# Kernel tuning notes

Hardware: AMD Instinct MI355X
Metric: run time of the kernel (lower is better)

Reference implementation:

```python
import jax, jax.numpy as jnp
import numpy as np

N, E, D, G, S, H = 100000, 1600000, 64, 1024, 4096, 128
BN_EPS = 1e-5


def setup_inputs() -> dict:
    key = jax.random.key(0)
    ks = jax.random.split(key, 24)
    x = jax.random.normal(ks[0], (N, D), jnp.float32)
    sid = jax.random.randint(ks[1], (N,), 0, S)
    x = x.at[:, 5].set(sid.astype(jnp.float32))  # column 5 holds integer substructure ids
    edge_index = jax.random.randint(ks[2], (2, E), 0, N, dtype=jnp.int32)
    batch = jnp.sort(jax.random.randint(ks[3], (N,), 0, G, dtype=jnp.int32))

    def lin(k, fan_in, shape):
        return jax.random.normal(k, shape, jnp.float32) / np.sqrt(fan_in)

    return {
        "x": x, "edge_index": edge_index, "batch": batch,
        # substructure attention net: Linear(D,64) -> tanh -> Linear(64,1,no bias)
        "w1": lin(ks[4], D, (D, 64)), "b1": jnp.zeros((64,), jnp.float32),
        "w2": lin(ks[5], 64, (64,)),
        "cw0": lin(ks[6], D + 1, (D + 1, H)), "cb0": jnp.zeros((H,), jnp.float32),
        "cw_rest": lin(ks[7], H, (3, H, H)), "cb_rest": jnp.zeros((3, H), jnp.float32),
        # BatchNorm1d (eval mode: running stats)
        "bn_gamma": jnp.ones((4, H), jnp.float32), "bn_beta": jnp.zeros((4, H), jnp.float32),
        "bn_mean": 0.1 * jax.random.normal(ks[8], (4, H), jnp.float32),
        "bn_var": jax.random.uniform(ks[9], (4, H), jnp.float32, 0.5, 1.5),
        # pred head: Linear(128,64) -> ELU -> Linear(64,1)
        "hw1": lin(ks[10], H, (H, 64)), "hb1": jnp.zeros((64,), jnp.float32),
        "hw2": lin(ks[11], 64, (64, 1)), "hb2": jnp.zeros((1,), jnp.float32),
    }


def _subst_attention(x, subst_ids, w1, b1, w2):
    ones = jnp.ones((x.shape[0],), x.dtype)
    cnt = jax.ops.segment_sum(ones, subst_ids, num_segments=S)
    sums = jax.ops.segment_sum(x, subst_ids, num_segments=S)
    means = sums / jnp.maximum(cnt, 1.0)[:, None]          # [S, D] per-substructure mean
    scores = jnp.tanh(means @ w1 + b1) @ w2                # [S]
    attn = jax.nn.softmax(scores, axis=0)                  # softmax over substructures
    return attn[subst_ids][:, None]                        # [N, 1] broadcast back to atoms


def _gcn(x, W, b, row, col, norm, n):
    h = x @ W                                              # [N, H]
    msg = h[row] * norm[:, None]                           # gather + scale  [E+N, H]
    return jax.ops.segment_sum(msg, col, num_segments=n) + b


def reference(x, edge_index, batch, w1, b1, w2, cw0, cb0, cw_rest, cb_rest,
              bn_gamma, bn_beta, bn_mean, bn_var, hw1, hb1, hw2, hb2):
    n = x.shape[0]
    subst_ids = jax.lax.stop_gradient(x[:, 5]).astype(jnp.int32)
    attn = _subst_attention(x, subst_ids, w1, b1, w2)
    h = jnp.concatenate([x, attn], axis=1)                 # [N, D+1]

    # add self loops, symmetric GCN normalization (as in PyG GCNConv)
    loops = jnp.arange(n, dtype=edge_index.dtype)
    row = jnp.concatenate([edge_index[0], loops])
    col = jnp.concatenate([edge_index[1], loops])
    deg = jax.ops.segment_sum(jnp.ones_like(row, dtype=h.dtype), col, num_segments=n)
    dinv = jax.lax.rsqrt(jnp.maximum(deg, 1.0))
    norm = dinv[row] * dinv[col]

    def bn(z, i):
        return (z - bn_mean[i]) * jax.lax.rsqrt(bn_var[i] + BN_EPS) * bn_gamma[i] + bn_beta[i]

    h = jax.nn.elu(bn(_gcn(h, cw0, cb0, row, col, norm, n), 0))
    for i in range(3):
        z = bn(_gcn(h, cw_rest[i], cb_rest[i], row, col, norm, n), i + 1)
        h = jax.nn.elu(z) if i < 2 else jax.nn.relu(z)

    # global mean pool over graphs
    gcnt = jax.ops.segment_sum(jnp.ones((n,), h.dtype), batch, num_segments=G)
    pooled = jax.ops.segment_sum(h, batch, num_segments=G) / jnp.maximum(gcnt, 1.0)[:, None]

    return jax.nn.elu(pooled @ hw1 + hb1) @ hw2 + hb2      # [G, 1]
```

## Files before the change

kernel.cpp:

```cpp
#include <hip/hip_runtime.h>
#include <math.h>

static constexpr int SS = 4096;
static constexpr int HH = 128;
static constexpr float EPS_BN = 1e-5f;

typedef __attribute__((ext_vector_type(8))) short bf16x8;
typedef __attribute__((ext_vector_type(4))) float f32x4;

__device__ inline unsigned short f2bf(float f) {
  unsigned int u = __float_as_uint(f);
  return (unsigned short)((u + 0x7fffu + ((u >> 16) & 1u)) >> 16);
}
__device__ inline float bflo(unsigned int u) { return __uint_as_float(u << 16); }
__device__ inline float bfhi(unsigned int u) { return __uint_as_float(u & 0xffff0000u); }


__device__ void wpack_body(const float* __restrict__ W, unsigned short* __restrict__ out,
                           int nkc, int idx) {
  if (idx >= 8 * nkc * 64) return;
  int lane = idx & 63;
  int kc = (idx >> 6) % nkc;
  int nt = idx / (64 * nkc);
  int colc = nt * 16 + (lane & 15);
  int k0 = kc * 32 + (lane >> 4) * 8;
  unsigned int w[4];
  #pragma unroll
  for (int i = 0; i < 4; ++i) {
    unsigned short a = f2bf(W[(size_t)(k0 + 2 * i) * 128 + colc]);
    unsigned short b = f2bf(W[(size_t)(k0 + 2 * i + 1) * 128 + colc]);
    w[i] = (unsigned int)a | ((unsigned int)b << 16);
  }
  *(uint4*)&out[(size_t)idx * 8] = make_uint4(w[0], w[1], w[2], w[3]);
}

__global__ __launch_bounds__(256)
void gcn_front1(const int* __restrict__ col, int* __restrict__ fill, int* __restrict__ pos,
                const float* __restrict__ x, float* __restrict__ cnt, float* __restrict__ sums,
                unsigned int* __restrict__ xh, const int* __restrict__ batch,
                int* __restrict__ gstart,
                const float* __restrict__ cw0, const float* __restrict__ cwr,
                unsigned short* __restrict__ wpk0, unsigned short* __restrict__ wpkr,
                const float* __restrict__ cb0, const float* __restrict__ cbr,
                const float* __restrict__ bng, const float* __restrict__ bnb,
                const float* __restrict__ bnm, const float* __restrict__ bnv,
                float* __restrict__ bnS, float* __restrict__ bnT,
                int n, int e, int G,
                int nbPos, int nbSub, int nbXb, int nbGb, int nbW0, int nbWr) {
  int b = blockIdx.x;
  int t = threadIdx.x;
  if (b < nbPos) {
    int i = b * 256 + t;
    if (i < e) pos[i] = atomicAdd(&fill[col[i]], 1);
    return;
  }
  b -= nbPos;
  if (b < nbSub) {
    int node = b * 4 + (t >> 6);
    int lane = t & 63;
    if (node >= n) return;
    const float* xr = x + (size_t)node * 64;
    float v = xr[lane];
    int sid = (int)__shfl(v, 5, 64);
    if (lane == 0) atomicAdd(&cnt[sid], 1.0f);
    atomicAdd(&sums[(size_t)sid * 64 + lane], v);
    return;
  }
  b -= nbSub;
  if (b < nbXb) {
    int i = b * 256 + t;
    if (i >= n * 32) return;
    int pr = i & 31;
    float2 v = *(const float2*)&x[(size_t)(i >> 5) * 64 + pr * 2];
    if (pr == 2) v.y = 0.f;
    xh[i] = (unsigned int)f2bf(v.x) | ((unsigned int)f2bf(v.y) << 16);
    return;
  }
  b -= nbXb;
  if (b < nbGb) {
    int g = b * 256 + t;
    if (g > G) return;
    if (g == G) { gstart[G] = n; return; }
    int lo = 0, hi = n;
    while (lo < hi) { int mid = (lo + hi) >> 1; if (batch[mid] < g) lo = mid + 1; else hi = mid; }
    gstart[g] = lo;
    return;
  }
  b -= nbGb;
  if (b < nbW0) { wpack_body(cw0, wpk0, 2, b * 256 + t); return; }
  b -= nbW0;
  if (b < 3 * nbWr) {
    int l = b / nbWr, bb = b % nbWr;
    wpack_body(cwr + (size_t)l * HH * HH, wpkr + (size_t)l * 8 * 4 * 64 * 8, 4, bb * 256 + t);
    return;
  }
  b -= 3 * nbWr;
  {
    int i = b * 256 + t;
    if (i >= 512) return;
    int l = i >> 7, c = i & 127;
    float S = rsqrtf(bnv[i] + EPS_BN) * bng[i];
    float bias = (l == 0) ? cb0[c] : cbr[(l - 1) * 128 + c];
    bnS[i] = S;
    bnT[i] = fmaf(bias - bnm[i], S, bnb[i]);
  }
}


__global__ void gcn_scores(const float* __restrict__ sums, const float* __restrict__ cnt,
                           const float* __restrict__ w1, const float* __restrict__ b1,
                           const float* __restrict__ w2, float* __restrict__ scores) {
  int s = blockIdx.x * 4 + (threadIdx.x >> 6);
  int j = threadIdx.x & 63;
  float r = 1.0f / fmaxf(cnt[s], 1.0f);
  const float* ss = sums + (size_t)s * 64;
  float acc = b1[j];
  #pragma unroll 8
  for (int d = 0; d < 64; ++d) acc = fmaf(ss[d] * r, w1[d * 64 + j], acc);
  float t = tanhf(acc) * w2[j];
  #pragma unroll
  for (int off = 32; off; off >>= 1) t += __shfl_down(t, off, 64);
  if (j == 0) scores[s] = t;
}

__global__ void gcn_softmax(float* __restrict__ sc) {
  int t = threadIdx.x;
  int wid = t >> 6;
  float v[4]; float m = -INFINITY;
  for (int i = 0; i < 4; ++i) { v[i] = sc[t + i * 1024]; m = fmaxf(m, v[i]); }
  for (int off = 32; off; off >>= 1) m = fmaxf(m, __shfl_xor(m, off, 64));
  __shared__ float wmax[16];
  if ((t & 63) == 0) wmax[wid] = m;
  __syncthreads();
  if (t == 0) { float mm = wmax[0]; for (int i = 1; i < 16; ++i) mm = fmaxf(mm, wmax[i]); wmax[0] = mm; }
  __syncthreads();
  float M = wmax[0];
  float s = 0.f;
  for (int i = 0; i < 4; ++i) { v[i] = expf(v[i] - M); s += v[i]; }
  for (int off = 32; off; off >>= 1) s += __shfl_xor(s, off, 64);
  __shared__ float wsum[16];
  if ((t & 63) == 0) wsum[wid] = s;
  __syncthreads();
  if (t == 0) { float ts = 0.f; for (int i = 0; i < 16; ++i) ts += wsum[i]; wsum[0] = ts; }
  __syncthreads();
  float inv = 1.0f / wsum[0];
  for (int i = 0; i < 4; ++i) sc[t + i * 1024] = v[i] * inv;
}


__global__ void gcn_scan1(const int* __restrict__ fill, int* __restrict__ rowstart,
                          int* __restrict__ bsum, float* __restrict__ dinv, int n) {
  __shared__ int tmp[1024];
  int t = threadIdx.x; int g = blockIdx.x * 1024 + t;
  int v = (g < n) ? fill[g] : 0;
  if (g < n) dinv[g] = rsqrtf((float)v + 1.0f);
  tmp[t] = v; __syncthreads();
  for (int off = 1; off < 1024; off <<= 1) {
    int a = (t >= off) ? tmp[t - off] : 0; __syncthreads();
    tmp[t] += a; __syncthreads();
  }
  if (g < n) rowstart[g] = tmp[t] - v;
  if (t == 1023) bsum[blockIdx.x] = tmp[t];
}

__global__ void gcn_scan2(int* __restrict__ bsum, int nb) {
  __shared__ int tmp[128];
  int t = threadIdx.x;
  int v = (t < nb) ? bsum[t] : 0;
  tmp[t] = v; __syncthreads();
  for (int off = 1; off < 128; off <<= 1) {
    int a = (t >= off) ? tmp[t - off] : 0; __syncthreads();
    tmp[t] += a; __syncthreads();
  }
  if (t < nb) bsum[t] = tmp[t] - v;
}

__global__ void gcn_scan3(int* __restrict__ rowstart, const int* __restrict__ bsum, int n, int e) {
  int g = blockIdx.x * 1024 + threadIdx.x;
  if (g < n) rowstart[g] += bsum[blockIdx.x];
  if (g == 0) rowstart[n] = e;
}


__global__ __launch_bounds__(256)
void gcn_front3(const float* __restrict__ x, const float* __restrict__ attn,
                float2* __restrict__ np,
                const int* __restrict__ row, const int* __restrict__ col,
                const int* __restrict__ pos, const int* __restrict__ rowstart,
                const float* __restrict__ dinv, int2* __restrict__ sedge,
                int n, int e, int nbNp) {
  int b = blockIdx.x;
  int t = threadIdx.x;
  if (b < nbNp) {
    int i = b * 256 + t;
    if (i >= n) return;
    int sid = (int)x[(size_t)i * 64 + 5];
    np[i] = make_float2((float)sid, attn[sid]);
    return;
  }
  b -= nbNp;
  int i = b * 256 + t;
  if (i >= e) return;
  int c = col[i], r = row[i];
  sedge[rowstart[c] + pos[i]] = make_int2(r, __float_as_int(dinv[r] * dinv[c]));
}


__global__ __launch_bounds__(256)
void gcn_layer_f(const unsigned short* __restrict__ hIn, const int2* __restrict__ sedge,
                 const int* __restrict__ rowstart, const float* __restrict__ dinv,
                 const unsigned short* __restrict__ Wpk,
                 const float* __restrict__ bnS, const float* __restrict__ bnT,
                 unsigned short* __restrict__ hOut, int relu, int n) {
  __shared__ unsigned short tile[4][16][136];
  int t = threadIdx.x;
  int wid = t >> 6, l = t & 63;
  int r = l & 15, kg = l >> 4;
  size_t row0w = (size_t)blockIdx.x * 64 + wid * 16;
  int noderaw = (int)row0w + r;
  bool valid = noderaw < n;
  int node = valid ? noderaw : n - 1;
  float di = dinv[node], d2 = di * di;
  const uint4* h4 = (const uint4*)hIn;
  float a[4][8];
  #pragma unroll
  for (int kc = 0; kc < 4; ++kc) {
    uint4 u = h4[(size_t)node * 16 + kc * 4 + kg];
    a[kc][0] = bflo(u.x) * d2; a[kc][1] = bfhi(u.x) * d2;
    a[kc][2] = bflo(u.y) * d2; a[kc][3] = bfhi(u.y) * d2;
    a[kc][4] = bflo(u.z) * d2; a[kc][5] = bfhi(u.z) * d2;
    a[kc][6] = bflo(u.w) * d2; a[kc][7] = bfhi(u.w) * d2;
  }
  int s_ = valid ? rowstart[node] : 0;
  int e_ = valid ? rowstart[node + 1] : 0;
  int2 se = (s_ < e_) ? sedge[s_] : make_int2(0, 0);
  for (int j = s_; j < e_; ++j) {
    int2 cur = se;
    if (j + 1 < e_) se = sedge[j + 1];
    float w = __int_as_float(cur.y);
    #pragma unroll
    for (int kc = 0; kc < 4; ++kc) {
      uint4 u = h4[(size_t)cur.x * 16 + kc * 4 + kg];
      a[kc][0] = fmaf(bflo(u.x), w, a[kc][0]); a[kc][1] = fmaf(bfhi(u.x), w, a[kc][1]);
      a[kc][2] = fmaf(bflo(u.y), w, a[kc][2]); a[kc][3] = fmaf(bfhi(u.y), w, a[kc][3]);
      a[kc][4] = fmaf(bflo(u.z), w, a[kc][4]); a[kc][5] = fmaf(bfhi(u.z), w, a[kc][5]);
      a[kc][6] = fmaf(bflo(u.w), w, a[kc][6]); a[kc][7] = fmaf(bfhi(u.w), w, a[kc][7]);
    }
  }
  bf16x8 af[4];
  #pragma unroll
  for (int kc = 0; kc < 4; ++kc) {
    uint4 pk;
    pk.x = (unsigned)f2bf(a[kc][0]) | ((unsigned)f2bf(a[kc][1]) << 16);
    pk.y = (unsigned)f2bf(a[kc][2]) | ((unsigned)f2bf(a[kc][3]) << 16);
    pk.z = (unsigned)f2bf(a[kc][4]) | ((unsigned)f2bf(a[kc][5]) << 16);
    pk.w = (unsigned)f2bf(a[kc][6]) | ((unsigned)f2bf(a[kc][7]) << 16);
    af[kc] = *(bf16x8*)&pk;
  }
  f32x4 acc[8];
  #pragma unroll
  for (int nt = 0; nt < 8; ++nt) acc[nt] = (f32x4){0.f, 0.f, 0.f, 0.f};
  const unsigned short* wp = Wpk + (size_t)l * 8;
  #pragma unroll
  for (int kc = 0; kc < 4; ++kc) {
    bf16x8 bf[8];
    #pragma unroll
    for (int nt = 0; nt < 8; ++nt)
      bf[nt] = *(const bf16x8*)(wp + (size_t)(nt * 4 + kc) * 512);
    #pragma unroll
    for (int nt = 0; nt < 8; ++nt)
      acc[nt] = __builtin_amdgcn_mfma_f32_16x16x32_bf16(af[kc], bf[nt], acc[nt], 0, 0, 0);
  }
  int colb = l & 15, rb = kg * 4;
  #pragma unroll
  for (int nt = 0; nt < 8; ++nt) {
    int c = nt * 16 + colb;
    float S = bnS[c], T = bnT[c];
    #pragma unroll
    for (int j = 0; j < 4; ++j) {
      float v = fmaf(acc[nt][j], S, T);
      v = relu ? fmaxf(v, 0.f) : (v > 0.f ? v : expf(v) - 1.f);
      tile[wid][rb + j][c] = f2bf(v);
    }
  }
  __syncthreads();
  #pragma unroll
  for (int i = 0; i < 4; ++i) {
    int m = i * 64 + l;
    int rr = m >> 4, chunk = m & 15;
    uint4 v = *(const uint4*)&tile[wid][rr][chunk * 8];
    *(uint4*)&hOut[(row0w + rr) * 128 + chunk * 8] = v;
  }
}


__global__ __launch_bounds__(256)
void gcn_layer0_f(const unsigned int* __restrict__ xh, const float2* __restrict__ np,
                  const int2* __restrict__ sedge, const int* __restrict__ rowstart,
                  const float* __restrict__ dinv, const unsigned short* __restrict__ Wpk0,
                  const float* __restrict__ cw0,
                  const float* __restrict__ bnS, const float* __restrict__ bnT,
                  unsigned short* __restrict__ hOut, int n) {
  __shared__ unsigned short tile[4][16][136];
  int t = threadIdx.x;
  int wid = t >> 6, l = t & 63;
  int r = l & 15, kg = l >> 4;
  size_t row0w = (size_t)blockIdx.x * 64 + wid * 16;
  int noderaw = (int)row0w + r;
  bool valid = noderaw < n;
  int node = valid ? noderaw : n - 1;
  float di = dinv[node], d2 = di * di;
  const uint4* x4 = (const uint4*)xh;
  float a[2][8];
  #pragma unroll
  for (int kc = 0; kc < 2; ++kc) {
    uint4 u = x4[(size_t)node * 8 + kc * 4 + kg];
    a[kc][0] = bflo(u.x) * d2; a[kc][1] = bfhi(u.x) * d2;
    a[kc][2] = bflo(u.y) * d2; a[kc][3] = bfhi(u.y) * d2;
    a[kc][4] = bflo(u.z) * d2; a[kc][5] = bfhi(u.z) * d2;
    a[kc][6] = bflo(u.w) * d2; a[kc][7] = bfhi(u.w) * d2;
  }
  float a5 = 0.f, a64 = 0.f;
  if (kg == 0) { float2 v = np[node]; a5 = d2 * v.x; a64 = d2 * v.y; }
  int s_ = valid ? rowstart[node] : 0;
  int e_ = valid ? rowstart[node + 1] : 0;
  int2 se = (s_ < e_) ? sedge[s_] : make_int2(0, 0);
  for (int j = s_; j < e_; ++j) {
    int2 cur = se;
    if (j + 1 < e_) se = sedge[j + 1];
    float w = __int_as_float(cur.y);
    #pragma unroll
    for (int kc = 0; kc < 2; ++kc) {
      uint4 u = x4[(size_t)cur.x * 8 + kc * 4 + kg];
      a[kc][0] = fmaf(bflo(u.x), w, a[kc][0]); a[kc][1] = fmaf(bfhi(u.x), w, a[kc][1]);
      a[kc][2] = fmaf(bflo(u.y), w, a[kc][2]); a[kc][3] = fmaf(bfhi(u.y), w, a[kc][3]);
      a[kc][4] = fmaf(bflo(u.z), w, a[kc][4]); a[kc][5] = fmaf(bfhi(u.z), w, a[kc][5]);
      a[kc][6] = fmaf(bflo(u.w), w, a[kc][6]); a[kc][7] = fmaf(bfhi(u.w), w, a[kc][7]);
    }
    if (kg == 0) {
      float2 v = np[cur.x];
      a5 = fmaf(v.x, w, a5);
      a64 = fmaf(v.y, w, a64);
    }
  }
  bf16x8 af[2];
  #pragma unroll
  for (int kc = 0; kc < 2; ++kc) {
    uint4 pk;
    pk.x = (unsigned)f2bf(a[kc][0]) | ((unsigned)f2bf(a[kc][1]) << 16);
    pk.y = (unsigned)f2bf(a[kc][2]) | ((unsigned)f2bf(a[kc][3]) << 16);
    pk.z = (unsigned)f2bf(a[kc][4]) | ((unsigned)f2bf(a[kc][5]) << 16);
    pk.w = (unsigned)f2bf(a[kc][6]) | ((unsigned)f2bf(a[kc][7]) << 16);
    af[kc] = *(bf16x8*)&pk;
  }
  f32x4 acc[8];
  #pragma unroll
  for (int nt = 0; nt < 8; ++nt) acc[nt] = (f32x4){0.f, 0.f, 0.f, 0.f};
  const unsigned short* wp = Wpk0 + (size_t)l * 8;
  #pragma unroll
  for (int kc = 0; kc < 2; ++kc) {
    bf16x8 bf[8];
    #pragma unroll
    for (int nt = 0; nt < 8; ++nt)
      bf[nt] = *(const bf16x8*)(wp + (size_t)(nt * 2 + kc) * 512);
    #pragma unroll
    for (int nt = 0; nt < 8; ++nt)
      acc[nt] = __builtin_amdgcn_mfma_f32_16x16x32_bf16(af[kc], bf[nt], acc[nt], 0, 0, 0);
  }
  int colb = l & 15, rb = kg * 4;
  float2 ax[4];
  #pragma unroll
  for (int j = 0; j < 4; ++j) {
    ax[j].x = __shfl(a5, rb + j, 64);
    ax[j].y = __shfl(a64, rb + j, 64);
  }
  #pragma unroll
  for (int nt = 0; nt < 8; ++nt) {
    int c = nt * 16 + colb;
    float w5 = cw0[5 * 128 + c], w64 = cw0[64 * 128 + c];
    float S = bnS[c], T = bnT[c];
    #pragma unroll
    for (int j = 0; j < 4; ++j) {
      float z = acc[nt][j] + ax[j].x * w5 + ax[j].y * w64;
      float v = fmaf(z, S, T);
      v = v > 0.f ? v : expf(v) - 1.f;
      tile[wid][rb + j][c] = f2bf(v);
    }
  }
  __syncthreads();
  #pragma unroll
  for (int i = 0; i < 4; ++i) {
    int m = i * 64 + l;
    int rr = m >> 4, chunk = m & 15;
    uint4 v = *(const uint4*)&tile[wid][rr][chunk * 8];
    *(uint4*)&hOut[(row0w + rr) * 128 + chunk * 8] = v;
  }
}


__global__ void gcn_pool2(const unsigned short* __restrict__ hB, const int* __restrict__ gstart,
                          float* __restrict__ pooled, int G) {
  int g = blockIdx.x * 4 + (threadIdx.x >> 6);
  int lane = threadIdx.x & 63;
  if (g >= G) return;
  int s = gstart[g], epos = gstart[g + 1];
  const unsigned int* h32 = (const unsigned int*)hB;
  float ax = 0.f, ay = 0.f;
  for (int i = s; i < epos; ++i) {
    unsigned int u = h32[(size_t)i * 64 + lane];
    ax += bflo(u);
    ay += bfhi(u);
  }
  float r = 1.0f / fmaxf((float)(epos - s), 1.0f);
  ((float2*)pooled)[(size_t)g * 64 + lane] = make_float2(ax * r, ay * r);
}

__global__ void gcn_head(const float* __restrict__ pooled,
                         const float* __restrict__ hw1, const float* __restrict__ hb1,
                         const float* __restrict__ hw2, const float* __restrict__ hb2,
                         float* __restrict__ out, int g) {
  int gi = blockIdx.x * 4 + (threadIdx.x >> 6);
  int j = threadIdx.x & 63;
  if (gi >= g) return;
  const float* p = pooled + (size_t)gi * 128;
  float acc = hb1[j];
  #pragma unroll 8
  for (int k = 0; k < 128; ++k) acc = fmaf(p[k], hw1[k * 64 + j], acc);
  float t = acc > 0.f ? acc : expf(acc) - 1.f;
  t *= hw2[j];
  #pragma unroll
  for (int off = 32; off; off >>= 1) t += __shfl_down(t, off, 64);
  if (j == 0) out[gi] = t + hb2[0];
}


extern "C" void kernel_launch(void* const* d_in, const int* in_sizes, int n_in,
                              void* d_out, int out_size, void* d_ws, size_t ws_size,
                              hipStream_t stream) {
  const float* x   = (const float*)d_in[0];
  const int*   ei  = (const int*)d_in[1];
  const int*   batch = (const int*)d_in[2];
  const float* w1  = (const float*)d_in[3];
  const float* b1  = (const float*)d_in[4];
  const float* w2  = (const float*)d_in[5];
  const float* cw0 = (const float*)d_in[6];
  const float* cb0 = (const float*)d_in[7];
  const float* cwr = (const float*)d_in[8];
  const float* cbr = (const float*)d_in[9];
  const float* bng = (const float*)d_in[10];
  const float* bnb = (const float*)d_in[11];
  const float* bnm = (const float*)d_in[12];
  const float* bnv = (const float*)d_in[13];
  const float* hw1 = (const float*)d_in[14];
  const float* hb1 = (const float*)d_in[15];
  const float* hw2 = (const float*)d_in[16];
  const float* hb2 = (const float*)d_in[17];
  float* out = (float*)d_out;
  (void)n_in; (void)ws_size;

  const int n = in_sizes[0] / 64;
  const int e = in_sizes[1] / 2;
  const int G = out_size;
  const int* row = ei;
  const int* col = ei + e;
  const int nb128 = (n + 127) / 128;
  const int n_pad = nb128 * 128;

  char* p = (char*)d_ws;
  auto take = [&](size_t bytes) { char* r = p; p += (bytes + 255) & ~(size_t)255; return r; };
  float* cnt    = (float*)take((size_t)SS * 4);
  float* sums   = (float*)take((size_t)SS * 64 * 4);
  float* attn   = (float*)take((size_t)SS * 4);
  float* dinv   = (float*)take((size_t)n * 4);
  int*   rowst  = (int*)take(((size_t)n + 1) * 4);
  int*   fill   = (int*)take((size_t)n * 4);
  int*   pos    = (int*)take((size_t)e * 4);
  int*   bsum   = (int*)take(128 * 4);
  int*   gstart = (int*)take(((size_t)G + 1) * 4);
  int2*  sedge  = (int2*)take((size_t)e * 8);
  float* pooled = (float*)take((size_t)G * HH * 4);
  float2* np    = (float2*)take((size_t)n * 8);
  unsigned int* xh = (unsigned int*)take((size_t)n * 32 * 4);
  unsigned short* hP0 = (unsigned short*)take((size_t)n_pad * HH * 2);
  unsigned short* hP1 = (unsigned short*)take((size_t)n_pad * HH * 2);
  unsigned short* wpk0 = (unsigned short*)take((size_t)8 * 2 * 64 * 8 * 2);
  unsigned short* wpkr = (unsigned short*)take((size_t)3 * 8 * 4 * 64 * 8 * 2);
  float* bnS    = (float*)take(4 * 128 * 4);
  float* bnT    = (float*)take(4 * 128 * 4);

  hipMemsetAsync(cnt, 0, (size_t)SS * 4, stream);
  hipMemsetAsync(sums, 0, (size_t)SS * 64 * 4, stream);
  hipMemsetAsync(fill, 0, (size_t)n * 4, stream);

  int nbPos = (e + 255) / 256;
  int nbSub = (n + 3) / 4;
  int nbXb  = (n * 32 + 255) / 256;
  int nbGb  = (G + 1 + 255) / 256;
  int nbW0 = 4, nbWr = 8, nbBnp = 2;
  int front1 = nbPos + nbSub + nbXb + nbGb + nbW0 + 3 * nbWr + nbBnp;
  gcn_front1<<<front1, 256, 0, stream>>>(col, fill, pos, x, cnt, sums, xh, batch, gstart,
      cw0, cwr, wpk0, wpkr, cb0, cbr, bng, bnb, bnm, bnv, bnS, bnT,
      n, e, G, nbPos, nbSub, nbXb, nbGb, nbW0, nbWr);

  gcn_scores<<<SS / 4, 256, 0, stream>>>(sums, cnt, w1, b1, w2, attn);
  gcn_softmax<<<1, 1024, 0, stream>>>(attn);

  int nb = (n + 1023) / 1024;
  gcn_scan1<<<nb, 1024, 0, stream>>>(fill, rowst, bsum, dinv, n);
  gcn_scan2<<<1, 128, 0, stream>>>(bsum, nb);
  gcn_scan3<<<nb, 1024, 0, stream>>>(rowst, bsum, n, e);

  int nbNp = (n + 255) / 256, nbSc = (e + 255) / 256;
  gcn_front3<<<nbNp + nbSc, 256, 0, stream>>>(x, attn, np, row, col, pos, rowst, dinv,
      sedge, n, e, nbNp);

  gcn_layer0_f<<<n_pad / 64, 256, 0, stream>>>(xh, np, sedge, rowst, dinv, wpk0, cw0,
      bnS, bnT, hP0, n);
  gcn_layer_f<<<n_pad / 64, 256, 0, stream>>>(hP0, sedge, rowst, dinv, wpkr,
      bnS + 128, bnT + 128, hP1, 0, n);
  gcn_layer_f<<<n_pad / 64, 256, 0, stream>>>(hP1, sedge, rowst, dinv,
      wpkr + (size_t)8 * 4 * 64 * 8, bnS + 256, bnT + 256, hP0, 0, n);
  gcn_layer_f<<<n_pad / 64, 256, 0, stream>>>(hP0, sedge, rowst, dinv,
      wpkr + (size_t)2 * 8 * 4 * 64 * 8, bnS + 384, bnT + 384, hP1, 1, n);

  gcn_pool2<<<(G + 3) / 4, 256, 0, stream>>>(hP1, gstart, pooled, G);
  gcn_head<<<(G + 3) / 4, 256, 0, stream>>>(pooled, hw1, hb1, hw2, hb2, out, G);
}
```

Measured before the change: 625.4 us.

## Unroll edge gathers by two, regroup front kernels, fuse pool with head

Moves the xh conversion, graph-start search, weight packing and BN-constant work out of the atomic-heavy first front kernel into the later front3 launch, with the edge scatter placed first. Unrolls the neighbour-gather loops in both layer kernels by two so two rows' loads are in flight at once, replacing the one-ahead prefetch. Fuses mean pooling and the prediction head into one kernel, dropping the pooled buffer and one launch. The unrolling raises register pressure, which may lower occupancy in the layer kernels.

```diff
diff --git a/kernel.cpp b/kernel.cpp
--- a/kernel.cpp
+++ b/kernel.cpp
@@ -16,37 +16,10 @@
 __device__ inline float bfhi(unsigned int u) { return __uint_as_float(u & 0xffff0000u); }
 
 
-__device__ void wpack_body(const float* __restrict__ W, unsigned short* __restrict__ out,
-                           int nkc, int idx) {
-  if (idx >= 8 * nkc * 64) return;
-  int lane = idx & 63;
-  int kc = (idx >> 6) % nkc;
-  int nt = idx / (64 * nkc);
-  int colc = nt * 16 + (lane & 15);
-  int k0 = kc * 32 + (lane >> 4) * 8;
-  unsigned int w[4];
-  #pragma unroll
-  for (int i = 0; i < 4; ++i) {
-    unsigned short a = f2bf(W[(size_t)(k0 + 2 * i) * 128 + colc]);
-    unsigned short b = f2bf(W[(size_t)(k0 + 2 * i + 1) * 128 + colc]);
-    w[i] = (unsigned int)a | ((unsigned int)b << 16);
-  }
-  *(uint4*)&out[(size_t)idx * 8] = make_uint4(w[0], w[1], w[2], w[3]);
-}
-
 __global__ __launch_bounds__(256)
 void gcn_front1(const int* __restrict__ col, int* __restrict__ fill, int* __restrict__ pos,
                 const float* __restrict__ x, float* __restrict__ cnt, float* __restrict__ sums,
-                unsigned int* __restrict__ xh, const int* __restrict__ batch,
-                int* __restrict__ gstart,
-                const float* __restrict__ cw0, const float* __restrict__ cwr,
-                unsigned short* __restrict__ wpk0, unsigned short* __restrict__ wpkr,
-                const float* __restrict__ cb0, const float* __restrict__ cbr,
-                const float* __restrict__ bng, const float* __restrict__ bnb,
-                const float* __restrict__ bnm, const float* __restrict__ bnv,
-                float* __restrict__ bnS, float* __restrict__ bnT,
-                int n, int e, int G,
-                int nbPos, int nbSub, int nbXb, int nbGb, int nbW0, int nbWr) {
+                int n, int e, int nbPos) {
   int b = blockIdx.x;
   int t = threadIdx.x;
   if (b < nbPos) {
@@ -55,7 +28,7 @@
     return;
   }
   b -= nbPos;
-  if (b < nbSub) {
+  {
     int node = b * 4 + (t >> 6);
     int lane = t & 63;
     if (node >= n) return;
@@ -64,45 +37,6 @@
     int sid = (int)__shfl(v, 5, 64);
     if (lane == 0) atomicAdd(&cnt[sid], 1.0f);
     atomicAdd(&sums[(size_t)sid * 64 + lane], v);
-    return;
-  }
-  b -= nbSub;
-  if (b < nbXb) {
-    int i = b * 256 + t;
-    if (i >= n * 32) return;
-    int pr = i & 31;
-    float2 v = *(const float2*)&x[(size_t)(i >> 5) * 64 + pr * 2];
-    if (pr == 2) v.y = 0.f;
-    xh[i] = (unsigned int)f2bf(v.x) | ((unsigned int)f2bf(v.y) << 16);
-    return;
-  }
-  b -= nbXb;
-  if (b < nbGb) {
-    int g = b * 256 + t;
-    if (g > G) return;
-    if (g == G) { gstart[G] = n; return; }
-    int lo = 0, hi = n;
-    while (lo < hi) { int mid = (lo + hi) >> 1; if (batch[mid] < g) lo = mid + 1; else hi = mid; }
-    gstart[g] = lo;
-    return;
-  }
-  b -= nbGb;
-  if (b < nbW0) { wpack_body(cw0, wpk0, 2, b * 256 + t); return; }
-  b -= nbW0;
-  if (b < 3 * nbWr) {
-    int l = b / nbWr, bb = b % nbWr;
-    wpack_body(cwr + (size_t)l * HH * HH, wpkr + (size_t)l * 8 * 4 * 64 * 8, 4, bb * 256 + t);
-    return;
-  }
-  b -= 3 * nbWr;
-  {
-    int i = b * 256 + t;
-    if (i >= 512) return;
-    int l = i >> 7, c = i & 127;
-    float S = rsqrtf(bnv[i] + EPS_BN) * bng[i];
-    float bias = (l == 0) ? cb0[c] : cbr[(l - 1) * 128 + c];
-    bnS[i] = S;
-    bnT[i] = fmaf(bias - bnm[i], S, bnb[i]);
   }
 }
 
@@ -182,15 +116,50 @@
 }
 
 
+__device__ void wpack_body(const float* __restrict__ W, unsigned short* __restrict__ out,
+                           int nkc, int idx) {
+  if (idx >= 8 * nkc * 64) return;
+  int lane = idx & 63;
+  int kc = (idx >> 6) % nkc;
+  int nt = idx / (64 * nkc);
+  int colc = nt * 16 + (lane & 15);
+  int k0 = kc * 32 + (lane >> 4) * 8;
+  unsigned int w[4];
+  #pragma unroll
+  for (int i = 0; i < 4; ++i) {
+    unsigned short a = f2bf(W[(size_t)(k0 + 2 * i) * 128 + colc]);
+    unsigned short b = f2bf(W[(size_t)(k0 + 2 * i + 1) * 128 + colc]);
+    w[i] = (unsigned int)a | ((unsigned int)b << 16);
+  }
+  *(uint4*)&out[(size_t)idx * 8] = make_uint4(w[0], w[1], w[2], w[3]);
+}
+
 __global__ __launch_bounds__(256)
 void gcn_front3(const float* __restrict__ x, const float* __restrict__ attn,
                 float2* __restrict__ np,
                 const int* __restrict__ row, const int* __restrict__ col,
                 const int* __restrict__ pos, const int* __restrict__ rowstart,
                 const float* __restrict__ dinv, int2* __restrict__ sedge,
-                int n, int e, int nbNp) {
+                unsigned int* __restrict__ xh, const int* __restrict__ batch,
+                int* __restrict__ gstart,
+                const float* __restrict__ cw0, const float* __restrict__ cwr,
+                unsigned short* __restrict__ wpk0, unsigned short* __restrict__ wpkr,
+                const float* __restrict__ cb0, const float* __restrict__ cbr,
+                const float* __restrict__ bng, const float* __restrict__ bnb,
+                const float* __restrict__ bnm, const float* __restrict__ bnv,
+                float* __restrict__ bnS, float* __restrict__ bnT,
+                int n, int e, int G,
+                int nbSc, int nbNp, int nbXb, int nbGb, int nbW0, int nbWr) {
   int b = blockIdx.x;
   int t = threadIdx.x;
+  if (b < nbSc) {
+    int i = b * 256 + t;
+    if (i >= e) return;
+    int c = col[i], r = row[i];
+    sedge[rowstart[c] + pos[i]] = make_int2(r, __float_as_int(dinv[r] * dinv[c]));
+    return;
+  }
+  b -= nbSc;
   if (b < nbNp) {
     int i = b * 256 + t;
     if (i >= n) return;
@@ -199,10 +168,43 @@
     return;
   }
   b -= nbNp;
-  int i = b * 256 + t;
-  if (i >= e) return;
-  int c = col[i], r = row[i];
-  sedge[rowstart[c] + pos[i]] = make_int2(r, __float_as_int(dinv[r] * dinv[c]));
+  if (b < nbXb) {
+    int i = b * 256 + t;
+    if (i >= n * 32) return;
+    int pr = i & 31;
+    float2 v = *(const float2*)&x[(size_t)(i >> 5) * 64 + pr * 2];
+    if (pr == 2) v.y = 0.f;
+    xh[i] = (unsigned int)f2bf(v.x) | ((unsigned int)f2bf(v.y) << 16);
+    return;
+  }
+  b -= nbXb;
+  if (b < nbGb) {
+    int g = b * 256 + t;
+    if (g > G) return;
+    if (g == G) { gstart[G] = n; return; }
+    int lo = 0, hi = n;
+    while (lo < hi) { int mid = (lo + hi) >> 1; if (batch[mid] < g) lo = mid + 1; else hi = mid; }
+    gstart[g] = lo;
+    return;
+  }
+  b -= nbGb;
+  if (b < nbW0) { wpack_body(cw0, wpk0, 2, b * 256 + t); return; }
+  b -= nbW0;
+  if (b < 3 * nbWr) {
+    int l = b / nbWr, bb = b % nbWr;
+    wpack_body(cwr + (size_t)l * HH * HH, wpkr + (size_t)l * 8 * 4 * 64 * 8, 4, bb * 256 + t);
+    return;
+  }
+  b -= 3 * nbWr;
+  {
+    int i = b * 256 + t;
+    if (i >= 512) return;
+    int l = i >> 7, c = i & 127;
+    float S = rsqrtf(bnv[i] + EPS_BN) * bng[i];
+    float bias = (l == 0) ? cb0[c] : cbr[(l - 1) * 128 + c];
+    bnS[i] = S;
+    bnT[i] = fmaf(bias - bnm[i], S, bnb[i]);
+  }
 }
 
 
@@ -233,18 +235,40 @@
   }
   int s_ = valid ? rowstart[node] : 0;
   int e_ = valid ? rowstart[node + 1] : 0;
-  int2 se = (s_ < e_) ? sedge[s_] : make_int2(0, 0);
-  for (int j = s_; j < e_; ++j) {
-    int2 cur = se;
-    if (j + 1 < e_) se = sedge[j + 1];
-    float w = __int_as_float(cur.y);
+  int j = s_;
+  for (; j + 2 <= e_; j += 2) {
+    int2 sA = sedge[j], sB = sedge[j + 1];
+    float wA = __int_as_float(sA.y), wB = __int_as_float(sB.y);
+    uint4 uA[4], uB[4];
+    #pragma unroll
+    for (int kc = 0; kc < 4; ++kc) uA[kc] = h4[(size_t)sA.x * 16 + kc * 4 + kg];
+    #pragma unroll
+    for (int kc = 0; kc < 4; ++kc) uB[kc] = h4[(size_t)sB.x * 16 + kc * 4 + kg];
     #pragma unroll
     for (int kc = 0; kc < 4; ++kc) {
-      uint4 u = h4[(size_t)cur.x * 16 + kc * 4 + kg];
-      a[kc][0] = fmaf(bflo(u.x), w, a[kc][0]); a[kc][1] = fmaf(bfhi(u.x), w, a[kc][1]);
-      a[kc][2] = fmaf(bflo(u.y), w, a[kc][2]); a[kc][3] = fmaf(bfhi(u.y), w, a[kc][3]);
-      a[kc][4] = fmaf(bflo(u.z), w, a[kc][4]); a[kc][5] = fmaf(bfhi(u.z), w, a[kc][5]);
-      a[kc][6] = fmaf(bflo(u.w), w, a[kc][6]); a[kc][7] = fmaf(bfhi(u.w), w, a[kc][7]);
+      a[kc][0] = fmaf(bflo(uA[kc].x), wA, a[kc][0]); a[kc][1] = fmaf(bfhi(uA[kc].x), wA, a[kc][1]);
+      a[kc][2] = fmaf(bflo(uA[kc].y), wA, a[kc][2]); a[kc][3] = fmaf(bfhi(uA[kc].y), wA, a[kc][3]);
+      a[kc][4] = fmaf(bflo(uA[kc].z), wA, a[kc][4]); a[kc][5] = fmaf(bfhi(uA[kc].z), wA, a[kc][5]);
+      a[kc][6] = fmaf(bflo(uA[kc].w), wA, a[kc][6]); a[kc][7] = fmaf(bfhi(uA[kc].w), wA, a[kc][7]);
+    }
+    #pragma unroll
+    for (int kc = 0; kc < 4; ++kc) {
+      a[kc][0] = fmaf(bflo(uB[kc].x), wB, a[kc][0]); a[kc][1] = fmaf(bfhi(uB[kc].x), wB, a[kc][1]);
+      a[kc][2] = fmaf(bflo(uB[kc].y), wB, a[kc][2]); a[kc][3] = fmaf(bfhi(uB[kc].y), wB, a[kc][3]);
+      a[kc][4] = fmaf(bflo(uB[kc].z), wB, a[kc][4]); a[kc][5] = fmaf(bfhi(uB[kc].z), wB, a[kc][5]);
+      a[kc][6] = fmaf(bflo(uB[kc].w), wB, a[kc][6]); a[kc][7] = fmaf(bfhi(uB[kc].w), wB, a[kc][7]);
+    }
+  }
+  if (j < e_) {
+    int2 sA = sedge[j];
+    float wA = __int_as_float(sA.y);
+    #pragma unroll
+    for (int kc = 0; kc < 4; ++kc) {
+      uint4 u = h4[(size_t)sA.x * 16 + kc * 4 + kg];
+      a[kc][0] = fmaf(bflo(u.x), wA, a[kc][0]); a[kc][1] = fmaf(bfhi(u.x), wA, a[kc][1]);
+      a[kc][2] = fmaf(bflo(u.y), wA, a[kc][2]); a[kc][3] = fmaf(bfhi(u.y), wA, a[kc][3]);
+      a[kc][4] = fmaf(bflo(u.z), wA, a[kc][4]); a[kc][5] = fmaf(bfhi(u.z), wA, a[kc][5]);
+      a[kc][6] = fmaf(bflo(u.w), wA, a[kc][6]); a[kc][7] = fmaf(bfhi(u.w), wA, a[kc][7]);
     }
   }
   bf16x8 af[4];
@@ -277,10 +301,10 @@
     int c = nt * 16 + colb;
     float S = bnS[c], T = bnT[c];
     #pragma unroll
-    for (int j = 0; j < 4; ++j) {
-      float v = fmaf(acc[nt][j], S, T);
+    for (int jj = 0; jj < 4; ++jj) {
+      float v = fmaf(acc[nt][jj], S, T);
       v = relu ? fmaxf(v, 0.f) : (v > 0.f ? v : expf(v) - 1.f);
-      tile[wid][rb + j][c] = f2bf(v);
+      tile[wid][rb + jj][c] = f2bf(v);
     }
   }
   __syncthreads();
@@ -324,23 +348,47 @@
   if (kg == 0) { float2 v = np[node]; a5 = d2 * v.x; a64 = d2 * v.y; }
   int s_ = valid ? rowstart[node] : 0;
   int e_ = valid ? rowstart[node + 1] : 0;
-  int2 se = (s_ < e_) ? sedge[s_] : make_int2(0, 0);
-  for (int j = s_; j < e_; ++j) {
-    int2 cur = se;
-    if (j + 1 < e_) se = sedge[j + 1];
-    float w = __int_as_float(cur.y);
+  int j = s_;
+  for (; j + 2 <= e_; j += 2) {
+    int2 sA = sedge[j], sB = sedge[j + 1];
+    float wA = __int_as_float(sA.y), wB = __int_as_float(sB.y);
+    uint4 uA[2], uB[2];
+    #pragma unroll
+    for (int kc = 0; kc < 2; ++kc) uA[kc] = x4[(size_t)sA.x * 8 + kc * 4 + kg];
+    #pragma unroll
+    for (int kc = 0; kc < 2; ++kc) uB[kc] = x4[(size_t)sB.x * 8 + kc * 4 + kg];
+    float2 vA, vB;
+    if (kg == 0) { vA = np[sA.x]; vB = np[sB.x]; }
     #pragma unroll
     for (int kc = 0; kc < 2; ++kc) {
-      uint4 u = x4[(size_t)cur.x * 8 + kc * 4 + kg];
-      a[kc][0] = fmaf(bflo(u.x), w, a[kc][0]); a[kc][1] = fmaf(bfhi(u.x), w, a[kc][1]);
-      a[kc][2] = fmaf(bflo(u.y), w, a[kc][2]); a[kc][3] = fmaf(bfhi(u.y), w, a[kc][3]);
-      a[kc][4] = fmaf(bflo(u.z), w, a[kc][4]); a[kc][5] = fmaf(bfhi(u.z), w, a[kc][5]);
-      a[kc][6] = fmaf(bflo(u.w), w, a[kc][6]); a[kc][7] = fmaf(bfhi(u.w), w, a[kc][7]);
+      a[kc][0] = fmaf(bflo(uA[kc].x), wA, a[kc][0]); a[kc][1] = fmaf(bfhi(uA[kc].x), wA, a[kc][1]);
+      a[kc][2] = fmaf(bflo(uA[kc].y), wA, a[kc][2]); a[kc][3] = fmaf(bfhi(uA[kc].y), wA, a[kc][3]);
+      a[kc][4] = fmaf(bflo(uA[kc].z), wA, a[kc][4]); a[kc][5] = fmaf(bfhi(uA[kc].z), wA, a[kc][5]);
+      a[kc][6] = fmaf(bflo(uA[kc].w), wA, a[kc][6]); a[kc][7] = fmaf(bfhi(uA[kc].w), wA, a[kc][7]);
+      a[kc][0] = fmaf(bflo(uB[kc].x), wB, a[kc][0]); a[kc][1] = fmaf(bfhi(uB[kc].x), wB, a[kc][1]);
+      a[kc][2] = fmaf(bflo(uB[kc].y), wB, a[kc][2]); a[kc][3] = fmaf(bfhi(uB[kc].y), wB, a[kc][3]);
+      a[kc][4] = fmaf(bflo(uB[kc].z), wB, a[kc][4]); a[kc][5] = fmaf(bfhi(uB[kc].z), wB, a[kc][5]);
+      a[kc][6] = fmaf(bflo(uB[kc].w), wB, a[kc][6]); a[kc][7] = fmaf(bfhi(uB[kc].w), wB, a[kc][7]);
     }
     if (kg == 0) {
-      float2 v = np[cur.x];
-      a5 = fmaf(v.x, w, a5);
-      a64 = fmaf(v.y, w, a64);
+      a5 = fmaf(vA.x, wA, a5); a64 = fmaf(vA.y, wA, a64);
+      a5 = fmaf(vB.x, wB, a5); a64 = fmaf(vB.y, wB, a64);
+    }
+  }
+  if (j < e_) {
+    int2 sA = sedge[j];
+    float wA = __int_as_float(sA.y);
+    #pragma unroll
+    for (int kc = 0; kc < 2; ++kc) {
+      uint4 u = x4[(size_t)sA.x * 8 + kc * 4 + kg];
+      a[kc][0] = fmaf(bflo(u.x), wA, a[kc][0]); a[kc][1] = fmaf(bfhi(u.x), wA, a[kc][1]);
+      a[kc][2] = fmaf(bflo(u.y), wA, a[kc][2]); a[kc][3] = fmaf(bfhi(u.y), wA, a[kc][3]);
+      a[kc][4] = fmaf(bflo(u.z), wA, a[kc][4]); a[kc][5] = fmaf(bfhi(u.z), wA, a[kc][5]);
+      a[kc][6] = fmaf(bflo(u.w), wA, a[kc][6]); a[kc][7] = fmaf(bfhi(u.w), wA, a[kc][7]);
+    }
+    if (kg == 0) {
+      float2 v = np[sA.x];
+      a5 = fmaf(v.x, wA, a5); a64 = fmaf(v.y, wA, a64);
     }
   }
   bf16x8 af[2];
@@ -370,9 +418,9 @@
   int colb = l & 15, rb = kg * 4;
   float2 ax[4];
   #pragma unroll
-  for (int j = 0; j < 4; ++j) {
-    ax[j].x = __shfl(a5, rb + j, 64);
-    ax[j].y = __shfl(a64, rb + j, 64);
+  for (int jj = 0; jj < 4; ++jj) {
+    ax[jj].x = __shfl(a5, rb + jj, 64);
+    ax[jj].y = __shfl(a64, rb + jj, 64);
   }
   #pragma unroll
   for (int nt = 0; nt < 8; ++nt) {
@@ -380,11 +428,11 @@
     float w5 = cw0[5 * 128 + c], w64 = cw0[64 * 128 + c];
     float S = bnS[c], T = bnT[c];
     #pragma unroll
-    for (int j = 0; j < 4; ++j) {
-      float z = acc[nt][j] + ax[j].x * w5 + ax[j].y * w64;
+    for (int jj = 0; jj < 4; ++jj) {
+      float z = acc[nt][jj] + ax[jj].x * w5 + ax[jj].y * w64;
       float v = fmaf(z, S, T);
       v = v > 0.f ? v : expf(v) - 1.f;
-      tile[wid][rb + j][c] = f2bf(v);
+      tile[wid][rb + jj][c] = f2bf(v);
     }
   }
   __syncthreads();
@@ -398,39 +446,40 @@
 }
 
 
-__global__ void gcn_pool2(const unsigned short* __restrict__ hB, const int* __restrict__ gstart,
-                          float* __restrict__ pooled, int G) {
-  int g = blockIdx.x * 4 + (threadIdx.x >> 6);
-  int lane = threadIdx.x & 63;
+__global__ __launch_bounds__(256)
+void gcn_poolhead(const unsigned short* __restrict__ hB, const int* __restrict__ gstart,
+                  const float* __restrict__ hw1, const float* __restrict__ hb1,
+                  const float* __restrict__ hw2, const float* __restrict__ hb2,
+                  float* __restrict__ out, int G) {
+  __shared__ float pl[4][128];
+  int wid = threadIdx.x >> 6, lane = threadIdx.x & 63;
+  int g = blockIdx.x * 4 + wid;
   if (g >= G) return;
-  int s = gstart[g], epos = gstart[g + 1];
+  int s = gstart[g], e = gstart[g + 1];
   const unsigned int* h32 = (const unsigned int*)hB;
   float ax = 0.f, ay = 0.f;
-  for (int i = s; i < epos; ++i) {
+  int i = s;
+  for (; i + 2 <= e; i += 2) {
+    unsigned int u0 = h32[(size_t)i * 64 + lane];
+    unsigned int u1 = h32[(size_t)(i + 1) * 64 + lane];
+    ax += bflo(u0) + bflo(u1);
+    ay += bfhi(u0) + bfhi(u1);
+  }
+  if (i < e) {
     unsigned int u = h32[(size_t)i * 64 + lane];
-    ax += bflo(u);
-    ay += bfhi(u);
-  }
-  float r = 1.0f / fmaxf((float)(epos - s), 1.0f);
-  ((float2*)pooled)[(size_t)g * 64 + lane] = make_float2(ax * r, ay * r);
-}
-
-__global__ void gcn_head(const float* __restrict__ pooled,
-                         const float* __restrict__ hw1, const float* __restrict__ hb1,
-                         const float* __restrict__ hw2, const float* __restrict__ hb2,
-                         float* __restrict__ out, int g) {
-  int gi = blockIdx.x * 4 + (threadIdx.x >> 6);
-  int j = threadIdx.x & 63;
-  if (gi >= g) return;
-  const float* p = pooled + (size_t)gi * 128;
-  float acc = hb1[j];
+    ax += bflo(u); ay += bfhi(u);
+  }
+  float r = 1.0f / fmaxf((float)(e - s), 1.0f);
+  pl[wid][lane * 2] = ax * r;
+  pl[wid][lane * 2 + 1] = ay * r;
+  float acc = hb1[lane];
   #pragma unroll 8
-  for (int k = 0; k < 128; ++k) acc = fmaf(p[k], hw1[k * 64 + j], acc);
-  float t = acc > 0.f ? acc : expf(acc) - 1.f;
-  t *= hw2[j];
-  #pragma unroll
-  for (int off = 32; off; off >>= 1) t += __shfl_down(t, off, 64);
-  if (j == 0) out[gi] = t + hb2[0];
+  for (int k = 0; k < 128; ++k) acc = fmaf(pl[wid][k], hw1[k * 64 + lane], acc);
+  float t2 = acc > 0.f ? acc : expf(acc) - 1.f;
+  t2 *= hw2[lane];
+  #pragma unroll
+  for (int off = 32; off; off >>= 1) t2 += __shfl_down(t2, off, 64);
+  if (lane == 0) out[g] = t2 + hb2[0];
 }
 
 
@@ -478,7 +527,6 @@
   int*   bsum   = (int*)take(128 * 4);
   int*   gstart = (int*)take(((size_t)G + 1) * 4);
   int2*  sedge  = (int2*)take((size_t)e * 8);
-  float* pooled = (float*)take((size_t)G * HH * 4);
   float2* np    = (float2*)take((size_t)n * 8);
   unsigned int* xh = (unsigned int*)take((size_t)n * 32 * 4);
   unsigned short* hP0 = (unsigned short*)take((size_t)n_pad * HH * 2);
@@ -494,13 +542,7 @@
 
   int nbPos = (e + 255) / 256;
   int nbSub = (n + 3) / 4;
-  int nbXb  = (n * 32 + 255) / 256;
-  int nbGb  = (G + 1 + 255) / 256;
-  int nbW0 = 4, nbWr = 8, nbBnp = 2;
-  int front1 = nbPos + nbSub + nbXb + nbGb + nbW0 + 3 * nbWr + nbBnp;
-  gcn_front1<<<front1, 256, 0, stream>>>(col, fill, pos, x, cnt, sums, xh, batch, gstart,
-      cw0, cwr, wpk0, wpkr, cb0, cbr, bng, bnb, bnm, bnv, bnS, bnT,
-      n, e, G, nbPos, nbSub, nbXb, nbGb, nbW0, nbWr);
+  gcn_front1<<<nbPos + nbSub, 256, 0, stream>>>(col, fill, pos, x, cnt, sums, n, e, nbPos);
 
   gcn_scores<<<SS / 4, 256, 0, stream>>>(sums, cnt, w1, b1, w2, attn);
   gcn_softmax<<<1, 1024, 0, stream>>>(attn);
@@ -510,9 +552,15 @@
   gcn_scan2<<<1, 128, 0, stream>>>(bsum, nb);
   gcn_scan3<<<nb, 1024, 0, stream>>>(rowst, bsum, n, e);
 
-  int nbNp = (n + 255) / 256, nbSc = (e + 255) / 256;
-  gcn_front3<<<nbNp + nbSc, 256, 0, stream>>>(x, attn, np, row, col, pos, rowst, dinv,
-      sedge, n, e, nbNp);
+  int nbSc = (e + 255) / 256;
+  int nbNp = (n + 255) / 256;
+  int nbXb = (n * 32 + 255) / 256;
+  int nbGb = (G + 1 + 255) / 256;
+  int nbW0 = 4, nbWr = 8, nbBnp = 2;
+  int front3 = nbSc + nbNp + nbXb + nbGb + nbW0 + 3 * nbWr + nbBnp;
+  gcn_front3<<<front3, 256, 0, stream>>>(x, attn, np, row, col, pos, rowst, dinv, sedge,
+      xh, batch, gstart, cw0, cwr, wpk0, wpkr, cb0, cbr, bng, bnb, bnm, bnv, bnS, bnT,
+      n, e, G, nbSc, nbNp, nbXb, nbGb, nbW0, nbWr);
 
   gcn_layer0_f<<<n_pad / 64, 256, 0, stream>>>(xh, np, sedge, rowst, dinv, wpk0, cw0,
       bnS, bnT, hP0, n);
@@ -523,6 +571,5 @@
   gcn_layer_f<<<n_pad / 64, 256, 0, stream>>>(hP0, sedge, rowst, dinv,
       wpkr + (size_t)2 * 8 * 4 * 64 * 8, bnS + 384, bnT + 384, hP1, 1, n);
 
-  gcn_pool2<<<(G + 3) / 4, 256, 0, stream>>>(hP1, gstart, pooled, G);
-  gcn_head<<<(G + 3) / 4, 256, 0, stream>>>(pooled, hw1, hb1, hw2, hb2, out, G);
-}
+  gcn_poolhead<<<(G + 3) / 4, 256, 0, stream>>>(hP1, gstart, hw1, hb1, hw2, hb2, out, G);
+}
```

After: 608.9 us. -2.6%, faster.
